# Kernel tuning notes

Measured on AMD Instinct MI355X. Metric: run time of the kernel, lower is better.

Reference implementation:

```python
import jax, jax.numpy as jnp
import numpy as np

PS = 8  # patch_size
EPS = 1e-5


def _layernorm(t, w, b):
    m = jnp.mean(t, axis=-1, keepdims=True)
    v = jnp.mean((t - m) ** 2, axis=-1, keepdims=True)
    return (t - m) * jax.lax.rsqrt(v + EPS) * w + b


def _to3d(t):  # B(HW)C -> BCHW
    B, N, C = t.shape
    H = W = int(np.sqrt(N))
    return t.reshape(B, H, W, C).transpose(0, 3, 1, 2)


def _to2d(t):  # BCHW -> B(HW)C
    B, C, H, W = t.shape
    return t.reshape(B, C, H * W).swapaxes(-1, -2)


def _block(t, ps=PS):  # BCHW -> [B, M, ps*ps, C] (dilated-grid blocking, as in torch code)
    B, C, H, W = t.shape
    t = t.reshape(B, C, ps, H // ps, ps, W // ps)
    t = t.transpose(0, 3, 5, 2, 4, 1)
    return t.reshape(B, (H * W) // (ps * ps), ps * ps, C)


def _unblock(t):  # inverse of _block
    B, M, N, C = t.shape
    Hb = Wb = int(np.sqrt(M))
    ps = int(np.sqrt(N))
    t = t.reshape(B, Hb, Wb, ps, ps, C)
    t = t.transpose(0, 5, 3, 1, 4, 2)
    return t.reshape(B, C, Hb * ps, Wb * ps)


def setup_inputs() -> dict:
    key = jax.random.key(0)
    ks = jax.random.split(key, 8)
    B, N, D, H = 8, 4096, 256, 8
    s = 1.0 / np.sqrt(D)
    return {
        "x": jax.random.normal(ks[0], (B, N, D), jnp.float32),
        "ln1_w": jnp.ones((D,), jnp.float32),
        "ln1_b": jnp.zeros((D,), jnp.float32),
        "q": jax.random.normal(ks[1], (H, D, D), jnp.float32) * s,
        "k": jax.random.normal(ks[2], (D, D), jnp.float32) * s,
        "v": jax.random.normal(ks[3], (D, D), jnp.float32) * s,
        "o": jax.random.normal(ks[4], (H, D, D), jnp.float32) * s,
        "ln2_w": jnp.ones((D,), jnp.float32),
        "ln2_b": jnp.zeros((D,), jnp.float32),
        "w1": jax.random.normal(ks[5], (D, D), jnp.float32) * s,
        "b1": jnp.zeros((D,), jnp.float32),
        "w2": jax.random.normal(ks[6], (D, D), jnp.float32) * s,
        "b2": jnp.zeros((D,), jnp.float32),
    }


def reference(x, ln1_w, ln1_b, q, k, v, o, ln2_w, ln2_b, w1, b1, w2, b2):
    # blocked input: [B, M, P, D], M = HW/ps^2, P = ps^2
    a = _block(_to3d(_layernorm(x, ln1_w, ln1_b)))
    nh = q.shape[0]
    Q = jnp.einsum('bmnd,hdk->bhmnk', a, q)
    Q1, Q2 = Q[:, : nh // 2], Q[:, nh // 2 :]
    K = jnp.einsum('bmnd,dk->bmnk', a, k)
    V = jnp.einsum('bmnd,dv->bmnv', a, v)
    # axis 1: attend across blocks (m) at fixed within-block position (y=n)
    s1 = jax.nn.softmax(jnp.einsum('bhxyk,bzyk->bhyxz', Q1, K), axis=-1)
    O1 = jnp.einsum('bhyxz,bzyv->bhxyv', s1, V)
    # axis 2: attend within block (n) at fixed block (x=m)
    s2 = jax.nn.softmax(jnp.einsum('bhxyk,bxzk->bhxyz', Q2, K), axis=-1)
    O2 = jnp.einsum('bhxyz,bxzv->bhxyv', s2, V)
    O = jnp.concatenate([O1, O2], axis=1)  # [B, H, M, P, D]
    # faithful to torch: 'bhmnd,hdv->bmnd' sums over h and v
    Z = jnp.einsum('bhmnd,hdv->bmnd', O, o)
    x = x + _to2d(_unblock(Z))
    h = _layernorm(x, ln2_w, ln2_b)
    mlp = jax.nn.relu(h @ w1 + b1) @ w2 + b2
    return x + mlp
```

## Files before the change

### kernel.cpp

```cpp
#include <hip/hip_runtime.h>

#define Bc   8
#define Tc   4096
#define Dc   256
#define EPSc 1e-5f

typedef _Float16 half_t;
typedef __attribute__((ext_vector_type(4))) _Float16 half4_t;
typedef __attribute__((ext_vector_type(8))) _Float16 frag8;
typedef __attribute__((ext_vector_type(4))) float f32x4;

#define MFMA_F16(a, b, c) __builtin_amdgcn_mfma_f32_16x16x32_f16((a), (b), (c), 0, 0, 0)

__global__ __launch_bounds__(256) void osum_kernel(const float* __restrict__ o, float* __restrict__ os) {
  int h = blockIdx.x, d = threadIdx.x;
  const float* row = o + ((size_t)h * 256 + d) * 256;
  float s = 0.f;
  #pragma unroll 8
  for (int v = 0; v < 256; v += 4) {
    float4 r4 = *(const float4*)&row[v];
    s += r4.x + r4.y + r4.z + r4.w;
  }
  os[h * 256 + d] = s;
}

__global__ __launch_bounds__(256) void prepM_kernel(const float* __restrict__ q,
                                                    const float* __restrict__ k,
                                                    half_t* __restrict__ Mt) {
  __shared__ float shK[32 * 260];
  __shared__ float shQ[32 * 260];
  int tid = threadIdx.x;
  int h = blockIdx.x >> 6, et = (blockIdx.x >> 3) & 7, dt = blockIdx.x & 7;
  const float* kbase = k + (size_t)(et * 32) * 256;
  const float* qbase = q + ((size_t)h * 256 + dt * 32) * 256;
  #pragma unroll
  for (int r = 0; r < 8; r++) {
    int f = r * 256 + tid;
    int row = f >> 6, c4 = (f & 63) * 4;
    *(float4*)&shK[row * 260 + c4] = *(const float4*)&kbase[(size_t)row * 256 + c4];
    *(float4*)&shQ[row * 260 + c4] = *(const float4*)&qbase[(size_t)row * 256 + c4];
  }
  __syncthreads();
  int e = tid & 31, dg = tid >> 5;
  const float* kr = &shK[e * 260];
  const float* q0 = &shQ[(dg * 4 + 0) * 260];
  const float* q1 = &shQ[(dg * 4 + 1) * 260];
  const float* q2 = &shQ[(dg * 4 + 2) * 260];
  const float* q3 = &shQ[(dg * 4 + 3) * 260];
  float a0 = 0.f, a1 = 0.f, a2 = 0.f, a3 = 0.f;
  #pragma unroll 4
  for (int kk = 0; kk < 256; kk += 4) {
    float4 kv = *(const float4*)&kr[kk];
    float4 v0 = *(const float4*)&q0[kk];
    float4 v1 = *(const float4*)&q1[kk];
    float4 v2 = *(const float4*)&q2[kk];
    float4 v3 = *(const float4*)&q3[kk];
    a0 += v0.x * kv.x + v0.y * kv.y + v0.z * kv.z + v0.w * kv.w;
    a1 += v1.x * kv.x + v1.y * kv.y + v1.z * kv.z + v1.w * kv.w;
    a2 += v2.x * kv.x + v2.y * kv.y + v2.z * kv.z + v2.w * kv.w;
    a3 += v3.x * kv.x + v3.y * kv.y + v3.z * kv.z + v3.w * kv.w;
  }
  half4_t outv;
  outv[0] = (half_t)a0; outv[1] = (half_t)a1; outv[2] = (half_t)a2; outv[3] = (half_t)a3;
  *(half4_t*)&Mt[((size_t)h * 256 + et * 32 + e) * 256 + dt * 32 + dg * 4] = outv;
}

__global__ __launch_bounds__(256) void prepT_kernel(const float* __restrict__ v,
                                                    const float* __restrict__ w1,
                                                    const float* __restrict__ w2,
                                                    half_t* vt, half_t* w1t, half_t* w2t) {
  int which = blockIdx.x >> 8, n = blockIdx.x & 255, d = threadIdx.x;
  const float* src = which == 0 ? v : (which == 1 ? w1 : w2);
  half_t* dst = which == 0 ? vt : (which == 1 ? w1t : w2t);
  dst[(size_t)n * 256 + d] = (half_t)src[(size_t)d * 256 + n];
}

__global__ __launch_bounds__(256) void ln1_kernel(
    const float* __restrict__ x, const float* __restrict__ w,
    const float* __restrict__ bia, half_t* __restrict__ aH) {
  int row  = blockIdx.x * 4 + (threadIdx.x >> 6);
  int lane = threadIdx.x & 63;
  float4 v = *(const float4*)&x[(size_t)row * 256 + lane * 4];
  float s  = v.x + v.y + v.z + v.w;
  float sq = v.x * v.x + v.y * v.y + v.z * v.z + v.w * v.w;
  #pragma unroll
  for (int off = 1; off < 64; off <<= 1) { s += __shfl_xor(s, off); sq += __shfl_xor(sq, off); }
  float mean = s * (1.f / 256), var = sq * (1.f / 256) - mean * mean;
  float r = rsqrtf(var + EPSc);
  float4 wv = *(const float4*)&w[lane * 4];
  float4 bv = *(const float4*)&bia[lane * 4];
  half4_t y;
  y[0] = (half_t)((v.x - mean) * r * wv.x + bv.x);
  y[1] = (half_t)((v.y - mean) * r * wv.y + bv.y);
  y[2] = (half_t)((v.z - mean) * r * wv.z + bv.z);
  y[3] = (half_t)((v.w - mean) * r * wv.w + bv.w);
  int bb = row >> 12, p = row & 4095, hh = p >> 6, ww = p & 63;
  int m = (hh & 7) * 8 + (ww & 7), n = (hh >> 3) * 8 + (ww >> 3);
  *(half4_t*)&aH[((size_t)((bb * 64 + m) * 64 + n)) * 256 + lane * 4] = y;
}

__global__ __launch_bounds__(256) void wgemm_kernel(
    const half_t* __restrict__ A, const half_t* __restrict__ Bt,
    const float* __restrict__ bias, float* __restrict__ outf,
    half_t* __restrict__ outh, int epi, int ldn, int mtiles) {
  __shared__ half_t shA[128 * 72];
  __shared__ half_t shB[128 * 72];
  int tid = threadIdx.x, lane = tid & 63, wave = tid >> 6;
  int l16 = lane & 15, quad = lane >> 4;
  int mtile = blockIdx.x % mtiles, ntile = blockIdx.x / mtiles;
  int r0 = mtile * 128, n0 = ntile * 128;
  int wm = (wave >> 1) * 64, wn = (wave & 1) * 64;
  f32x4 acc[4][4];
  #pragma unroll
  for (int mt = 0; mt < 4; mt++)
    #pragma unroll
    for (int nt = 0; nt < 4; nt++) acc[mt][nt] = (f32x4){0.f, 0.f, 0.f, 0.f};
  for (int kb = 0; kb < 256; kb += 64) {
    if (kb) __syncthreads();
    #pragma unroll
    for (int rr = 0; rr < 4; rr++) {
      int idx = rr * 256 + tid;
      int row = idx >> 3, c8 = (idx & 7) * 8;
      *(frag8*)&shA[row * 72 + c8] = *(const frag8*)&A[(size_t)(r0 + row) * 256 + kb + c8];
      *(frag8*)&shB[row * 72 + c8] = *(const frag8*)&Bt[(size_t)(n0 + row) * 256 + kb + c8];
    }
    __syncthreads();
    #pragma unroll
    for (int kh = 0; kh < 2; kh++) {
      int ko = kh * 32 + quad * 8;
      frag8 af[4], bf[4];
      #pragma unroll
      for (int mt = 0; mt < 4; mt++) af[mt] = *(const frag8*)&shA[(wm + mt * 16 + l16) * 72 + ko];
      #pragma unroll
      for (int nt = 0; nt < 4; nt++) bf[nt] = *(const frag8*)&shB[(wn + nt * 16 + l16) * 72 + ko];
      #pragma unroll
      for (int mt = 0; mt < 4; mt++)
        #pragma unroll
        for (int nt = 0; nt < 4; nt++) acc[mt][nt] = MFMA_F16(af[mt], bf[nt], acc[mt][nt]);
    }
  }
  #pragma unroll
  for (int mt = 0; mt < 4; mt++)
    #pragma unroll
    for (int nt = 0; nt < 4; nt++)
      #pragma unroll
      for (int r = 0; r < 4; r++) {
        int row = r0 + wm + mt * 16 + quad * 4 + r;
        int col = n0 + wn + nt * 16 + l16;
        float vv = acc[mt][nt][r];
        if (epi) vv += bias[col];
        if (epi == 1) vv = fmaxf(vv, 0.f);
        size_t idx = (size_t)row * ldn + col;
        if (epi == 2) outf[idx] = vv + outf[idx];
        else          outh[idx] = (half_t)vv;
      }
}

__global__ __launch_bounds__(256, 2) void attn_kernel(
    const half_t* __restrict__ aH, const half_t* __restrict__ Mt,
    const half_t* __restrict__ vt, const float* __restrict__ osum,
    half_t* __restrict__ Z0, half_t* __restrict__ Z1) {
  __shared__ half_t shA[64 * 264];
  __shared__ half_t shU[64 * 264 + 64 * 72];
  half_t* shVT = shU;
  half_t* shW  = shU;
  half_t* shP  = shU + 64 * 264;
  int tid = threadIdx.x, lane = tid & 63, w = tid >> 6;
  int l16 = lane & 15, quad = lane >> 4;
  int g = blockIdx.x;
  int mode = g >> 9, gg = g & 511, b = gg >> 6, slice = gg & 63;
  int hbase = mode * 4;
  half_t* Z = mode ? Z1 : Z0;

  #pragma unroll
  for (int i = 0; i < 8; i++) {
    int slot = i * 256 + tid;
    int z = slot >> 5, c8 = (slot & 31) * 8;
    size_t rz = mode ? ((size_t)(b * 64 + slice) * 64 + z) : ((size_t)(b * 64 + z) * 64 + slice);
    *(frag8*)&shA[z * 264 + c8] = *(const frag8*)&aH[rz * 256 + c8];
  }
  __syncthreads();

  #pragma unroll
  for (int dth = 0; dth < 2; dth++) {
    f32x4 vacc[2][4];
    #pragma unroll
    for (int dt2 = 0; dt2 < 2; dt2++)
      #pragma unroll
      for (int zt = 0; zt < 4; zt++) vacc[dt2][zt] = (f32x4){0.f, 0.f, 0.f, 0.f};
    #pragma unroll
    for (int ks = 0; ks < 8; ks++) {
      int k0 = ks * 32 + quad * 8;
      frag8 vf0 = *(const frag8*)&vt[(size_t)(w * 64 + dth * 32 +  0 + l16) * 256 + k0];
      frag8 vf1 = *(const frag8*)&vt[(size_t)(w * 64 + dth * 32 + 16 + l16) * 256 + k0];
      frag8 bfr[4];
      #pragma unroll
      for (int zt = 0; zt < 4; zt++)
        bfr[zt] = *(const frag8*)&shA[(zt * 16 + l16) * 264 + k0];
      #pragma unroll
      for (int zt = 0; zt < 4; zt++) {
        vacc[0][zt] = MFMA_F16(vf0, bfr[zt], vacc[0][zt]);
        vacc[1][zt] = MFMA_F16(vf1, bfr[zt], vacc[1][zt]);
      }
    }
    #pragma unroll
    for (int dt2 = 0; dt2 < 2; dt2++)
      #pragma unroll
      for (int zt = 0; zt < 4; zt++)
        #pragma unroll
        for (int r = 0; r < 4; r++)
          shVT[(w * 64 + dth * 32 + dt2 * 16 + quad * 4 + r) * 72 + zt * 16 + l16] = (half_t)vacc[dt2][zt][r];
  }
  __syncthreads();

  frag8 vtreg[4][2];
  #pragma unroll
  for (int dt = 0; dt < 4; dt++)
    #pragma unroll
    for (int ks = 0; ks < 2; ks++)
      vtreg[dt][ks] = *(const frag8*)&shVT[(w * 64 + dt * 16 + l16) * 72 + ks * 32 + quad * 8];

  float osv[4][4];
  #pragma unroll
  for (int hh = 0; hh < 4; hh++)
    #pragma unroll
    for (int dt = 0; dt < 4; dt++)
      osv[hh][dt] = osum[(hbase + hh) * 256 + w * 64 + dt * 16 + l16];

  f32x4 zacc[4][4];
  #pragma unroll
  for (int mf = 0; mf < 4; mf++)
    #pragma unroll
    for (int dt = 0; dt < 4; dt++) zacc[mf][dt] = (f32x4){0.f, 0.f, 0.f, 0.f};
  __syncthreads();

  #pragma unroll
  for (int hh = 0; hh < 4; hh++) {
    const half_t* Mth = Mt + (size_t)(hbase + hh) * 65536;
    #pragma unroll
    for (int eh = 0; eh < 2; eh++) {
      f32x4 wacc[2][4];
      #pragma unroll
      for (int et2 = 0; et2 < 2; et2++)
        #pragma unroll
        for (int mf = 0; mf < 4; mf++) wacc[et2][mf] = (f32x4){0.f, 0.f, 0.f, 0.f};
      #pragma unroll
      for (int ks = 0; ks < 8; ks++) {
        int k0 = ks * 32 + quad * 8;
        frag8 bf0 = *(const frag8*)&Mth[(size_t)(w * 64 + eh * 32 +  0 + l16) * 256 + k0];
        frag8 bf1 = *(const frag8*)&Mth[(size_t)(w * 64 + eh * 32 + 16 + l16) * 256 + k0];
        frag8 af[4];
        #pragma unroll
        for (int mf = 0; mf < 4; mf++) af[mf] = *(const frag8*)&shA[(mf * 16 + l16) * 264 + k0];
        #pragma unroll
        for (int mf = 0; mf < 4; mf++) {
          wacc[0][mf] = MFMA_F16(af[mf], bf0, wacc[0][mf]);
          wacc[1][mf] = MFMA_F16(af[mf], bf1, wacc[1][mf]);
        }
      }
      #pragma unroll
      for (int et2 = 0; et2 < 2; et2++)
        #pragma unroll
        for (int mf = 0; mf < 4; mf++)
          #pragma unroll
          for (int r = 0; r < 4; r++)
            shW[(mf * 16 + quad * 4 + r) * 264 + w * 64 + eh * 32 + et2 * 16 + l16] = (half_t)wacc[et2][mf][r];
    }
    __syncthreads();
    {
      f32x4 sacc[4];
      #pragma unroll
      for (int zt = 0; zt < 4; zt++) sacc[zt] = (f32x4){0.f, 0.f, 0.f, 0.f};
      #pragma unroll
      for (int ks = 0; ks < 8; ks++) {
        int k0 = ks * 32 + quad * 8;
        frag8 wf = *(const frag8*)&shW[(w * 16 + l16) * 264 + k0];
        #pragma unroll
        for (int zt = 0; zt < 4; zt++) {
          frag8 kf = *(const frag8*)&shA[(zt * 16 + l16) * 264 + k0];
          sacc[zt] = MFMA_F16(wf, kf, sacc[zt]);
        }
      }
      #pragma unroll
      for (int r = 0; r < 4; r++) {
        float mx = fmaxf(fmaxf(sacc[0][r], sacc[1][r]), fmaxf(sacc[2][r], sacc[3][r]));
        #pragma unroll
        for (int off = 1; off < 16; off <<= 1) mx = fmaxf(mx, __shfl_xor(mx, off));
        float e0 = __expf(sacc[0][r] - mx), e1 = __expf(sacc[1][r] - mx);
        float e2 = __expf(sacc[2][r] - mx), e3 = __expf(sacc[3][r] - mx);
        float sum = e0 + e1 + e2 + e3;
        #pragma unroll
        for (int off = 1; off < 16; off <<= 1) sum += __shfl_xor(sum, off);
        float inv = 1.f / sum;
        int m = w * 16 + quad * 4 + r;
        shP[m * 72 + l16 +  0] = (half_t)(e0 * inv);
        shP[m * 72 + l16 + 16] = (half_t)(e1 * inv);
        shP[m * 72 + l16 + 32] = (half_t)(e2 * inv);
        shP[m * 72 + l16 + 48] = (half_t)(e3 * inv);
      }
    }
    __syncthreads();
    #pragma unroll
    for (int mf = 0; mf < 4; mf++) {
      frag8 pf0 = *(const frag8*)&shP[(mf * 16 + l16) * 72 +  0 + quad * 8];
      frag8 pf1 = *(const frag8*)&shP[(mf * 16 + l16) * 72 + 32 + quad * 8];
      #pragma unroll
      for (int dt = 0; dt < 4; dt++) {
        f32x4 oacc = (f32x4){0.f, 0.f, 0.f, 0.f};
        oacc = MFMA_F16(pf0, vtreg[dt][0], oacc);
        oacc = MFMA_F16(pf1, vtreg[dt][1], oacc);
        #pragma unroll
        for (int r = 0; r < 4; r++) zacc[mf][dt][r] += oacc[r] * osv[hh][dt];
      }
    }
  }

  #pragma unroll
  for (int mf = 0; mf < 4; mf++)
    #pragma unroll
    for (int dt = 0; dt < 4; dt++)
      #pragma unroll
      for (int r = 0; r < 4; r++)
        shA[(mf * 16 + quad * 4 + r) * 264 + w * 64 + dt * 16 + l16] = (half_t)zacc[mf][dt][r];
  __syncthreads();
  #pragma unroll
  for (int i = 0; i < 8; i++) {
    int slot = i * 256 + tid;
    int grow = slot >> 5, c8 = (slot & 31) * 8;
    size_t zrow = mode ? ((size_t)(b * 64 + slice) * 64 + grow) : ((size_t)(b * 64 + grow) * 64 + slice);
    *(frag8*)&Z[zrow * 256 + c8] = *(const frag8*)&shA[grow * 264 + c8];
  }
}

__global__ __launch_bounds__(256) void ln2_kernel(
    const float* __restrict__ x, const half_t* __restrict__ Z0, const half_t* __restrict__ Z1,
    const float* __restrict__ w, const float* __restrict__ bia,
    float* __restrict__ x2out, half_t* __restrict__ hH) {
  int row  = blockIdx.x * 4 + (threadIdx.x >> 6);
  int lane = threadIdx.x & 63;
  size_t base = (size_t)row * 256 + lane * 4;
  int bb = row >> 12, p = row & 4095, hh = p >> 6, ww = p & 63;
  int m = (hh & 7) * 8 + (ww & 7), n = (hh >> 3) * 8 + (ww >> 3);
  size_t zbase = ((size_t)((bb * 64 + m) * 64 + n)) * 256 + lane * 4;
  float4 xv = *(const float4*)&x[base];
  half4_t zv0 = *(const half4_t*)&Z0[zbase];
  half4_t zv1 = *(const half4_t*)&Z1[zbase];
  float4 v;
  v.x = xv.x + (float)zv0[0] + (float)zv1[0];
  v.y = xv.y + (float)zv0[1] + (float)zv1[1];
  v.z = xv.z + (float)zv0[2] + (float)zv1[2];
  v.w = xv.w + (float)zv0[3] + (float)zv1[3];
  float s  = v.x + v.y + v.z + v.w;
  float sq = v.x * v.x + v.y * v.y + v.z * v.z + v.w * v.w;
  #pragma unroll
  for (int off = 1; off < 64; off <<= 1) { s += __shfl_xor(s, off); sq += __shfl_xor(sq, off); }
  float mean = s * (1.f / 256), var = sq * (1.f / 256) - mean * mean;
  float r = rsqrtf(var + EPSc);
  float4 wv = *(const float4*)&w[lane * 4];
  float4 bv = *(const float4*)&bia[lane * 4];
  *(float4*)&x2out[base] = v;
  half4_t y;
  y[0] = (half_t)((v.x - mean) * r * wv.x + bv.x);
  y[1] = (half_t)((v.y - mean) * r * wv.y + bv.y);
  y[2] = (half_t)((v.z - mean) * r * wv.z + bv.z);
  y[3] = (half_t)((v.w - mean) * r * wv.w + bv.w);
  *(half4_t*)&hH[base] = y;
}

extern "C" void kernel_launch(void* const* d_in, const int* in_sizes, int n_in,
                              void* d_out, int out_size, void* d_ws, size_t ws_size,
                              hipStream_t stream) {
  (void)in_sizes; (void)n_in; (void)out_size; (void)ws_size;
  const float* x    = (const float*)d_in[0];
  const float* ln1w = (const float*)d_in[1];
  const float* ln1b = (const float*)d_in[2];
  const float* q    = (const float*)d_in[3];
  const float* k    = (const float*)d_in[4];
  const float* v    = (const float*)d_in[5];
  const float* o    = (const float*)d_in[6];
  const float* ln2w = (const float*)d_in[7];
  const float* ln2b = (const float*)d_in[8];
  const float* w1   = (const float*)d_in[9];
  const float* b1   = (const float*)d_in[10];
  const float* w2   = (const float*)d_in[11];
  const float* b2   = (const float*)d_in[12];
  float* out = (float*)d_out;

  const size_t ROWS = (size_t)Bc * Tc;
  const size_t ELTS = ROWS * Dc;
  const size_t MB16 = ELTS * sizeof(half_t);
  char* ws = (char*)d_ws;
  float*  osumB = (float*)ws;
  half_t* Mt    = (half_t*)(ws + (64 << 10));
  half_t* vt    = (half_t*)(ws + (64 << 10) + (1 << 20));
  half_t* w1t   = (half_t*)(ws + (64 << 10) + (1 << 20) + (128 << 10));
  half_t* w2t   = (half_t*)(ws + (64 << 10) + (1 << 20) + (256 << 10));
  half_t* aH    = (half_t*)(ws + (2 << 20));
  half_t* Zb0   = (half_t*)(ws + (2 << 20) + MB16);
  half_t* Zb1   = (half_t*)(ws + (2 << 20) + 2 * MB16);
  half_t* hH    = aH;
  half_t* tH    = Zb1;

  osum_kernel <<<8,   256, 0, stream>>>(o, osumB);
  prepM_kernel<<<512, 256, 0, stream>>>(q, k, Mt);
  prepT_kernel<<<768, 256, 0, stream>>>(v, w1, w2, vt, w1t, w2t);
  ln1_kernel  <<<ROWS / 4, 256, 0, stream>>>(x, ln1w, ln1b, aH);
  attn_kernel <<<1024, 256, 0, stream>>>(aH, Mt, vt, osumB, Zb0, Zb1);
  ln2_kernel  <<<ROWS / 4, 256, 0, stream>>>(x, Zb0, Zb1, ln2w, ln2b, out, hH);
  wgemm_kernel<<<512, 256, 0, stream>>>(hH, w1t, b1, nullptr, tH, 1, 256, 256);
  wgemm_kernel<<<512, 256, 0, stream>>>(tH, w2t, b2, out, nullptr, 2, 256, 256);
}
```

Baseline: 316.5 us.

## Fuse residual add, LayerNorm2 and both MLP GEMMs into one kernel

Replaces the ln2 kernel and the two separate wgemm launches with a single mlp_kernel. Each block handles 32 rows: it computes the residual and LN2 into LDS, then runs the first GEMM with bias and ReLU into LDS, then the second GEMM with bias and residual straight to the output. This removes the global round trips for hH, tH and the intermediate x2 written to out, plus two launches. In exchange, weight fragments are read directly from global/L2 without LDS staging and each block reuses them across only 32 rows, so GEMM efficiency may drop.

```diff
diff --git a/kernel.cpp b/kernel.cpp
--- a/kernel.cpp
+++ b/kernel.cpp
@@ -99,63 +99,6 @@
   *(half4_t*)&aH[((size_t)((bb * 64 + m) * 64 + n)) * 256 + lane * 4] = y;
 }
 
-__global__ __launch_bounds__(256) void wgemm_kernel(
-    const half_t* __restrict__ A, const half_t* __restrict__ Bt,
-    const float* __restrict__ bias, float* __restrict__ outf,
-    half_t* __restrict__ outh, int epi, int ldn, int mtiles) {
-  __shared__ half_t shA[128 * 72];
-  __shared__ half_t shB[128 * 72];
-  int tid = threadIdx.x, lane = tid & 63, wave = tid >> 6;
-  int l16 = lane & 15, quad = lane >> 4;
-  int mtile = blockIdx.x % mtiles, ntile = blockIdx.x / mtiles;
-  int r0 = mtile * 128, n0 = ntile * 128;
-  int wm = (wave >> 1) * 64, wn = (wave & 1) * 64;
-  f32x4 acc[4][4];
-  #pragma unroll
-  for (int mt = 0; mt < 4; mt++)
-    #pragma unroll
-    for (int nt = 0; nt < 4; nt++) acc[mt][nt] = (f32x4){0.f, 0.f, 0.f, 0.f};
-  for (int kb = 0; kb < 256; kb += 64) {
-    if (kb) __syncthreads();
-    #pragma unroll
-    for (int rr = 0; rr < 4; rr++) {
-      int idx = rr * 256 + tid;
-      int row = idx >> 3, c8 = (idx & 7) * 8;
-      *(frag8*)&shA[row * 72 + c8] = *(const frag8*)&A[(size_t)(r0 + row) * 256 + kb + c8];
-      *(frag8*)&shB[row * 72 + c8] = *(const frag8*)&Bt[(size_t)(n0 + row) * 256 + kb + c8];
-    }
-    __syncthreads();
-    #pragma unroll
-    for (int kh = 0; kh < 2; kh++) {
-      int ko = kh * 32 + quad * 8;
-      frag8 af[4], bf[4];
-      #pragma unroll
-      for (int mt = 0; mt < 4; mt++) af[mt] = *(const frag8*)&shA[(wm + mt * 16 + l16) * 72 + ko];
-      #pragma unroll
-      for (int nt = 0; nt < 4; nt++) bf[nt] = *(const frag8*)&shB[(wn + nt * 16 + l16) * 72 + ko];
-      #pragma unroll
-      for (int mt = 0; mt < 4; mt++)
-        #pragma unroll
-        for (int nt = 0; nt < 4; nt++) acc[mt][nt] = MFMA_F16(af[mt], bf[nt], acc[mt][nt]);
-    }
-  }
-  #pragma unroll
-  for (int mt = 0; mt < 4; mt++)
-    #pragma unroll
-    for (int nt = 0; nt < 4; nt++)
-      #pragma unroll
-      for (int r = 0; r < 4; r++) {
-        int row = r0 + wm + mt * 16 + quad * 4 + r;
-        int col = n0 + wn + nt * 16 + l16;
-        float vv = acc[mt][nt][r];
-        if (epi) vv += bias[col];
-        if (epi == 1) vv = fmaxf(vv, 0.f);
-        size_t idx = (size_t)row * ldn + col;
-        if (epi == 2) outf[idx] = vv + outf[idx];
-        else          outh[idx] = (half_t)vv;
-      }
-}
-
 __global__ __launch_bounds__(256, 2) void attn_kernel(
     const half_t* __restrict__ aH, const half_t* __restrict__ Mt,
     const half_t* __restrict__ vt, const float* __restrict__ osum,
@@ -332,39 +275,118 @@
   }
 }
 
-__global__ __launch_bounds__(256) void ln2_kernel(
+__global__ __launch_bounds__(256, 2) void mlp_kernel(
     const float* __restrict__ x, const half_t* __restrict__ Z0, const half_t* __restrict__ Z1,
-    const float* __restrict__ w, const float* __restrict__ bia,
-    float* __restrict__ x2out, half_t* __restrict__ hH) {
-  int row  = blockIdx.x * 4 + (threadIdx.x >> 6);
-  int lane = threadIdx.x & 63;
-  size_t base = (size_t)row * 256 + lane * 4;
-  int bb = row >> 12, p = row & 4095, hh = p >> 6, ww = p & 63;
-  int m = (hh & 7) * 8 + (ww & 7), n = (hh >> 3) * 8 + (ww >> 3);
-  size_t zbase = ((size_t)((bb * 64 + m) * 64 + n)) * 256 + lane * 4;
-  float4 xv = *(const float4*)&x[base];
-  half4_t zv0 = *(const half4_t*)&Z0[zbase];
-  half4_t zv1 = *(const half4_t*)&Z1[zbase];
-  float4 v;
-  v.x = xv.x + (float)zv0[0] + (float)zv1[0];
-  v.y = xv.y + (float)zv0[1] + (float)zv1[1];
-  v.z = xv.z + (float)zv0[2] + (float)zv1[2];
-  v.w = xv.w + (float)zv0[3] + (float)zv1[3];
-  float s  = v.x + v.y + v.z + v.w;
-  float sq = v.x * v.x + v.y * v.y + v.z * v.z + v.w * v.w;
-  #pragma unroll
-  for (int off = 1; off < 64; off <<= 1) { s += __shfl_xor(s, off); sq += __shfl_xor(sq, off); }
-  float mean = s * (1.f / 256), var = sq * (1.f / 256) - mean * mean;
-  float r = rsqrtf(var + EPSc);
-  float4 wv = *(const float4*)&w[lane * 4];
-  float4 bv = *(const float4*)&bia[lane * 4];
-  *(float4*)&x2out[base] = v;
-  half4_t y;
-  y[0] = (half_t)((v.x - mean) * r * wv.x + bv.x);
-  y[1] = (half_t)((v.y - mean) * r * wv.y + bv.y);
-  y[2] = (half_t)((v.z - mean) * r * wv.z + bv.z);
-  y[3] = (half_t)((v.w - mean) * r * wv.w + bv.w);
-  *(half4_t*)&hH[base] = y;
+    const float* __restrict__ lw, const float* __restrict__ lb,
+    const half_t* __restrict__ w1t, const float* __restrict__ b1,
+    const half_t* __restrict__ w2t, const float* __restrict__ b2,
+    float* __restrict__ out) {
+  __shared__ float  shV[32 * 260];
+  __shared__ half_t shH[32 * 264];
+  __shared__ half_t shHH[32 * 264];
+  int tid = threadIdx.x, lane = tid & 63, w = tid >> 6;
+  int l16 = lane & 15, quad = lane >> 4;
+  int row0 = blockIdx.x * 32;
+
+  #pragma unroll
+  for (int i = 0; i < 8; i++) {
+    int rl = w * 8 + i;
+    int row = row0 + rl;
+    size_t base = (size_t)row * 256 + lane * 4;
+    int bb = row >> 12, p = row & 4095, hh = p >> 6, ww = p & 63;
+    int m = (hh & 7) * 8 + (ww & 7), n = (hh >> 3) * 8 + (ww >> 3);
+    size_t zbase = ((size_t)((bb * 64 + m) * 64 + n)) * 256 + lane * 4;
+    float4 xv = *(const float4*)&x[base];
+    half4_t zv0 = *(const half4_t*)&Z0[zbase];
+    half4_t zv1 = *(const half4_t*)&Z1[zbase];
+    float4 v;
+    v.x = xv.x + (float)zv0[0] + (float)zv1[0];
+    v.y = xv.y + (float)zv0[1] + (float)zv1[1];
+    v.z = xv.z + (float)zv0[2] + (float)zv1[2];
+    v.w = xv.w + (float)zv0[3] + (float)zv1[3];
+    *(float4*)&shV[rl * 260 + lane * 4] = v;
+    float s  = v.x + v.y + v.z + v.w;
+    float sq = v.x * v.x + v.y * v.y + v.z * v.z + v.w * v.w;
+    #pragma unroll
+    for (int off = 1; off < 64; off <<= 1) { s += __shfl_xor(s, off); sq += __shfl_xor(sq, off); }
+    float mean = s * (1.f / 256), var = sq * (1.f / 256) - mean * mean;
+    float r = rsqrtf(var + EPSc);
+    float4 wv = *(const float4*)&lw[lane * 4];
+    float4 bv = *(const float4*)&lb[lane * 4];
+    half4_t y;
+    y[0] = (half_t)((v.x - mean) * r * wv.x + bv.x);
+    y[1] = (half_t)((v.y - mean) * r * wv.y + bv.y);
+    y[2] = (half_t)((v.z - mean) * r * wv.z + bv.z);
+    y[3] = (half_t)((v.w - mean) * r * wv.w + bv.w);
+    *(half4_t*)&shH[rl * 264 + lane * 4] = y;
+  }
+  __syncthreads();
+
+  {
+    f32x4 acc[2][4];
+    #pragma unroll
+    for (int mf = 0; mf < 2; mf++)
+      #pragma unroll
+      for (int nt = 0; nt < 4; nt++) acc[mf][nt] = (f32x4){0.f, 0.f, 0.f, 0.f};
+    #pragma unroll
+    for (int ks = 0; ks < 8; ks++) {
+      int k0 = ks * 32 + quad * 8;
+      frag8 af[2], bf[4];
+      #pragma unroll
+      for (int mf = 0; mf < 2; mf++) af[mf] = *(const frag8*)&shH[(mf * 16 + l16) * 264 + k0];
+      #pragma unroll
+      for (int nt = 0; nt < 4; nt++)
+        bf[nt] = *(const frag8*)&w1t[(size_t)(w * 64 + nt * 16 + l16) * 256 + k0];
+      #pragma unroll
+      for (int mf = 0; mf < 2; mf++)
+        #pragma unroll
+        for (int nt = 0; nt < 4; nt++) acc[mf][nt] = MFMA_F16(af[mf], bf[nt], acc[mf][nt]);
+    }
+    #pragma unroll
+    for (int mf = 0; mf < 2; mf++)
+      #pragma unroll
+      for (int nt = 0; nt < 4; nt++)
+        #pragma unroll
+        for (int r = 0; r < 4; r++) {
+          int rr = mf * 16 + quad * 4 + r, col = w * 64 + nt * 16 + l16;
+          float vv = acc[mf][nt][r] + b1[col];
+          vv = fmaxf(vv, 0.f);
+          shHH[rr * 264 + col] = (half_t)vv;
+        }
+  }
+  __syncthreads();
+
+  {
+    f32x4 acc[2][4];
+    #pragma unroll
+    for (int mf = 0; mf < 2; mf++)
+      #pragma unroll
+      for (int nt = 0; nt < 4; nt++) acc[mf][nt] = (f32x4){0.f, 0.f, 0.f, 0.f};
+    #pragma unroll
+    for (int ks = 0; ks < 8; ks++) {
+      int k0 = ks * 32 + quad * 8;
+      frag8 af[2], bf[4];
+      #pragma unroll
+      for (int mf = 0; mf < 2; mf++) af[mf] = *(const frag8*)&shHH[(mf * 16 + l16) * 264 + k0];
+      #pragma unroll
+      for (int nt = 0; nt < 4; nt++)
+        bf[nt] = *(const frag8*)&w2t[(size_t)(w * 64 + nt * 16 + l16) * 256 + k0];
+      #pragma unroll
+      for (int mf = 0; mf < 2; mf++)
+        #pragma unroll
+        for (int nt = 0; nt < 4; nt++) acc[mf][nt] = MFMA_F16(af[mf], bf[nt], acc[mf][nt]);
+    }
+    #pragma unroll
+    for (int mf = 0; mf < 2; mf++)
+      #pragma unroll
+      for (int nt = 0; nt < 4; nt++)
+        #pragma unroll
+        for (int r = 0; r < 4; r++) {
+          int rr = mf * 16 + quad * 4 + r, col = w * 64 + nt * 16 + l16;
+          float vv = acc[mf][nt][r] + b2[col];
+          out[(size_t)(row0 + rr) * 256 + col] = vv + shV[rr * 260 + col];
+        }
+  }
 }
 
 extern "C" void kernel_launch(void* const* d_in, const int* in_sizes, int n_in,
@@ -398,15 +420,11 @@
   half_t* aH    = (half_t*)(ws + (2 << 20));
   half_t* Zb0   = (half_t*)(ws + (2 << 20) + MB16);
   half_t* Zb1   = (half_t*)(ws + (2 << 20) + 2 * MB16);
-  half_t* hH    = aH;
-  half_t* tH    = Zb1;
 
   osum_kernel <<<8,   256, 0, stream>>>(o, osumB);
   prepM_kernel<<<512, 256, 0, stream>>>(q, k, Mt);
   prepT_kernel<<<768, 256, 0, stream>>>(v, w1, w2, vt, w1t, w2t);
   ln1_kernel  <<<ROWS / 4, 256, 0, stream>>>(x, ln1w, ln1b, aH);
   attn_kernel <<<1024, 256, 0, stream>>>(aH, Mt, vt, osumB, Zb0, Zb1);
-  ln2_kernel  <<<ROWS / 4, 256, 0, stream>>>(x, Zb0, Zb1, ln2w, ln2b, out, hH);
-  wgemm_kernel<<<512, 256, 0, stream>>>(hH, w1t, b1, nullptr, tH, 1, 256, 256);
-  wgemm_kernel<<<512, 256, 0, stream>>>(tH, w2t, b2, out, nullptr, 2, 256, 256);
-}
+  mlp_kernel  <<<ROWS / 32, 256, 0, stream>>>(x, Zb0, Zb1, ln2w, ln2b, w1t, b1, w2t, b2, out);
+}
```

Result: faster. 276.6 us (-12.6%).
